# Kernel tuning notes

Measured on AMD Instinct MI355X. Metric: run time of the kernel, lower is better.

## Reference

```python
import jax, jax.numpy as jnp
import numpy as np

B, H, D, K, V, M = 64, 32, 4096, 128, 128, 4095

def setup_inputs() -> dict:
    key = jax.random.key(0)
    ks = jax.random.split(key, 7)
    return {
        "x": jax.random.normal(ks[0], (B, D), dtype=jnp.float32),
        "prev_K": jax.random.normal(ks[1], (B, M, K), dtype=jnp.float32),
        "prev_V": jax.random.normal(ks[2], (B, M, V), dtype=jnp.float32),
        "Wq": jax.random.normal(ks[3], (H, D, K), dtype=jnp.float32),
        "Wk": jax.random.normal(ks[4], (D, K), dtype=jnp.float32),
        "Wv": jax.random.normal(ks[5], (D, V), dtype=jnp.float32),
        "Wo": jax.random.normal(ks[6], (H, V, D), dtype=jnp.float32),
    }

def reference(x, prev_K, prev_V, Wq, Wk, Wv, Wo):
    # Projections
    q = jnp.einsum('bd,hdk->bhk', x, Wq)            # [b,h,k]
    k_new = jnp.einsum('bd,dk->bk', x, Wk)          # [b,k]
    v_new = jnp.einsum('bd,dv->bv', x, Wv)          # [b,v]
    Kc = jnp.concatenate([prev_K, k_new[:, None, :]], axis=1)  # [b,m+1,k]
    Vc = jnp.concatenate([prev_V, v_new[:, None, :]], axis=1)  # [b,m+1,v]
    # Shared-KV attention (MQA)
    logits = jnp.einsum('bhk,bmk->bhm', q, Kc)
    weights = jax.nn.softmax(logits, axis=-1)
    o = jnp.einsum('bhm,bmv->bhv', weights, Vc)
    y = jnp.einsum('bhv,hvd->bd', o, Wo)
    return (y, Kc, Vc)
```

## Files before the change

kernel.cpp:

```cpp
#include <hip/hip_runtime.h>
#include <stdint.h>

#define B_  64
#define H_  32
#define D_  4096
#define KD  128
#define VD  128
#define M_  4095
#define M1_ 4096
#define NCHUNK 32
#define LOG2E 1.44269504088896f

#define WS_P      0ull
#define WS_Q      4456448ull
#define WS_STATS  4718592ull
#define WS_O      4849664ull
#define WS_OPART  5111808ull

#define WAITV(n) asm volatile("s_waitcnt vmcnt(" #n ")" ::: "memory")
#define WAITVL(n) asm volatile("s_waitcnt vmcnt(" #n ") lgkmcnt(0)" ::: "memory")
#define WAITL()  asm volatile("s_waitcnt lgkmcnt(0)" ::: "memory")
#define BAR()    __builtin_amdgcn_s_barrier()

typedef __attribute__((address_space(3))) char lds_char;
typedef const __attribute__((address_space(1))) char glb_char;

__global__ __launch_bounds__(256) void k_proj_partial(
    const float* __restrict__ x, const float* __restrict__ Wq,
    const float* __restrict__ Wk, const float* __restrict__ Wv,
    float* __restrict__ P) {
  __shared__ float xs[64][256];
  const int dc = blockIdx.x;
  const int hx = blockIdx.y;
  const int t  = threadIdx.x;
  const float* xsrc = x + dc * 256;
  #pragma unroll
  for (int j = 0; j < 16; ++j) {
    int f = t + 256 * j;
    int row = f >> 6, c4 = f & 63;
    *(float4*)&xs[row][c4 * 4] =
        *(const float4*)(xsrc + (size_t)row * D_ + c4 * 4);
  }
  __syncthreads();
  const int bq = t >> 4;
  const int kg = t & 15;
  const int b0 = bq * 4;
  const float* W = (hx < H_) ? (Wq + (size_t)hx * D_ * KD)
                             : ((hx == H_) ? Wk : Wv);
  const float* wp = W + (size_t)(dc * 256) * KD + kg * 8;
  float acc[4][8];
  #pragma unroll
  for (int i = 0; i < 4; ++i)
    #pragma unroll
    for (int j = 0; j < 8; ++j) acc[i][j] = 0.f;
  #pragma unroll 8
  for (int d = 0; d < 256; ++d) {
    float4 w0 = *(const float4*)(wp + (size_t)d * KD);
    float4 w1 = *(const float4*)(wp + (size_t)d * KD + 4);
    float xv[4];
    #pragma unroll
    for (int i = 0; i < 4; ++i) xv[i] = xs[b0 + i][d];
    #pragma unroll
    for (int i = 0; i < 4; ++i) {
      acc[i][0] += xv[i] * w0.x; acc[i][1] += xv[i] * w0.y;
      acc[i][2] += xv[i] * w0.z; acc[i][3] += xv[i] * w0.w;
      acc[i][4] += xv[i] * w1.x; acc[i][5] += xv[i] * w1.y;
      acc[i][6] += xv[i] * w1.z; acc[i][7] += xv[i] * w1.w;
    }
  }
  #pragma unroll
  for (int i = 0; i < 4; ++i) {
    size_t base = ((size_t)(dc * 64 + b0 + i) * 34 + hx) * KD + kg * 8;
    *(float4*)&P[base]     = make_float4(acc[i][0], acc[i][1], acc[i][2], acc[i][3]);
    *(float4*)&P[base + 4] = make_float4(acc[i][4], acc[i][5], acc[i][6], acc[i][7]);
  }
}

__global__ __launch_bounds__(256) void k_proj_reduce(
    const float* __restrict__ P, float* __restrict__ q,
    float* __restrict__ Kc, float* __restrict__ Vc) {
  int i = blockIdx.x * 256 + threadIdx.x;
  int k = i & 127;
  int hx = (i >> 7) % 34;
  int b = i / (128 * 34);
  float s = 0.f;
  #pragma unroll
  for (int dc = 0; dc < 16; ++dc)
    s += P[(size_t)dc * (64 * 34 * 128) + (size_t)(b * 34 + hx) * 128 + k];
  if (hx < H_)       q[((size_t)b * H_ + hx) * KD + k] = s;
  else if (hx == H_) Kc[((size_t)b * M1_ + M_) * KD + k] = s;
  else               Vc[((size_t)b * M1_ + M_) * VD + k] = s;
}

__device__ __forceinline__ void stage_issue(
    const float* src, const float* app_row, float* lbuf, int m_lo, int t) {
  const int wb = t & ~63;
  #pragma unroll
  for (int j = 0; j < 4; ++j) {
    int f = j * 256 + t;
    int r = f >> 5, p = f & 31;
    int m = m_lo + r;
    int g4 = p ^ (r & 7);
    const float* gp = (m < M_) ? (src + (size_t)m * 128 + g4 * 4)
                               : (app_row + g4 * 4);
    __builtin_amdgcn_global_load_lds(
        (glb_char*)gp, (lds_char*)(lbuf + (size_t)(j * 256 + wb) * 4),
        16, 0, 0);
  }
}

__device__ __forceinline__ void copy_out(
    const float* lbuf, float* dst, int m_lo, int t) {
  const int r = t >> 3;
  const int m = m_lo + r;
  float* drow = dst + (size_t)m * 128;
  #pragma unroll
  for (int jj = 0; jj < 4; ++jj) {
    int g4 = (t & 7) + jj * 8;
    int p = g4 ^ (r & 7);
    float4 v = *(const float4*)&lbuf[(r * 32 + p) * 4];
    *(float4*)(drow + g4 * 4) = v;
  }
}

__global__ __launch_bounds__(256, 2) void k_flash(
    const float* __restrict__ prevK, const float* __restrict__ prevV,
    const float* __restrict__ q, float* __restrict__ Kc, float* __restrict__ Vc,
    float* __restrict__ o_part, float* __restrict__ stats) {
  __shared__ float buf[2][32 * 128];
  __shared__ float qs[32][128];
  __shared__ float wl[128 * 36];
  const int chunk = blockIdx.x;
  const int b = blockIdx.y;
  const int t = threadIdx.x;
  const int m0 = chunk * 128;

  const float* kbase = prevK + (size_t)b * M_ * KD;
  const float* vbase = prevV + (size_t)b * M_ * VD;
  const float* kapp  = Kc + ((size_t)b * M1_ + M_) * KD;
  const float* vapp  = Vc + ((size_t)b * M1_ + M_) * VD;
  float* kc = Kc + (size_t)b * M1_ * KD;
  float* vc = Vc + (size_t)b * M1_ * VD;

  const float* qsrc = q + (size_t)b * H_ * KD;
  float4 qv[4];
  #pragma unroll
  for (int j = 0; j < 4; ++j) {
    int f = j * 256 + t;
    qv[j] = *(const float4*)(qsrc + (size_t)(f >> 5) * KD + (f & 31) * 4);
  }
  stage_issue(kbase, kapp, buf[0], m0, t);
  #pragma unroll
  for (int j = 0; j < 4; ++j) {
    int f = j * 256 + t;
    *(float4*)&qs[f >> 5][(f & 31) * 4] = qv[j];
  }

  const int mg = t & 15, hg = t >> 4, h0 = hg * 2;
  const int v4 = t & 31, hoct = t >> 5, h0v = hoct * 4;

  float4 a0 = {0,0,0,0}, a1 = {0,0,0,0}, a2 = {0,0,0,0}, a3 = {0,0,0,0};

#define LOGITS_TILE(S, BUFI)                                                  \
  {                                                                           \
    const float* lb = buf[BUFI];                                              \
    float c00 = 0.f, c01 = 0.f, c10 = 0.f, c11 = 0.f;                         \
    const int sw = (mg & 7);                                                  \
    _Pragma("unroll 4")                                                       \
    for (int k4 = 0; k4 < 32; ++k4) {                                         \
      int p = (k4 ^ sw) * 4;                                                  \
      float4 qa = *(const float4*)&qs[h0][k4 * 4];                            \
      float4 qb = *(const float4*)&qs[h0 + 1][k4 * 4];                        \
      float4 k0v = *(const float4*)&lb[mg * 128 + p];                         \
      float4 k1v = *(const float4*)&lb[(mg + 16) * 128 + p];                  \
      c00 += qa.x*k0v.x + qa.y*k0v.y + qa.z*k0v.z + qa.w*k0v.w;               \
      c01 += qa.x*k1v.x + qa.y*k1v.y + qa.z*k1v.z + qa.w*k1v.w;               \
      c10 += qb.x*k0v.x + qb.y*k0v.y + qb.z*k0v.z + qb.w*k0v.w;               \
      c11 += qb.x*k1v.x + qb.y*k1v.y + qb.z*k1v.z + qb.w*k1v.w;               \
    }                                                                         \
    wl[((S) * 32 + mg) * 36 + h0]          = c00;                             \
    wl[((S) * 32 + mg + 16) * 36 + h0]     = c01;                             \
    wl[((S) * 32 + mg) * 36 + h0 + 1]      = c10;                             \
    wl[((S) * 32 + mg + 16) * 36 + h0 + 1] = c11;                             \
  }

#define PV_TILE(S, BUFI)                                                      \
  {                                                                           \
    const float* lb = buf[BUFI];                                              \
    _Pragma("unroll 4")                                                       \
    for (int mm = 0; mm < 32; ++mm) {                                         \
      int p = (v4 ^ (mm & 7)) * 4;                                            \
      float4 gv = *(const float4*)&lb[mm * 128 + p];                          \
      float4 w4 = *(const float4*)&wl[((S) * 32 + mm) * 36 + h0v];            \
      a0.x += w4.x*gv.x; a0.y += w4.x*gv.y; a0.z += w4.x*gv.z; a0.w += w4.x*gv.w; \
      a1.x += w4.y*gv.x; a1.y += w4.y*gv.y; a1.z += w4.y*gv.z; a1.w += w4.y*gv.w; \
      a2.x += w4.z*gv.x; a2.y += w4.z*gv.y; a2.z += w4.z*gv.z; a2.w += w4.z*gv.w; \
      a3.x += w4.w*gv.x; a3.y += w4.w*gv.y; a3.z += w4.w*gv.z; a3.w += w4.w*gv.w; \
    }                                                                         \
  }

  stage_issue(kbase, kapp, buf[1], m0 + 32, t);
  WAITVL(4); BAR();
  LOGITS_TILE(0, 0);
  copy_out(buf[0], kc, m0, t);
  WAITL(); BAR();
  stage_issue(kbase, kapp, buf[0], m0 + 64, t);
  WAITVL(8); BAR();
  LOGITS_TILE(1, 1);
  copy_out(buf[1], kc, m0 + 32, t);
  WAITL(); BAR();
  stage_issue(kbase, kapp, buf[1], m0 + 96, t);
  WAITVL(8); BAR();
  LOGITS_TILE(2, 0);
  copy_out(buf[0], kc, m0 + 64, t);
  WAITL(); BAR();
  stage_issue(vbase, vapp, buf[0], m0, t);
  WAITVL(8); BAR();
  LOGITS_TILE(3, 1);
  copy_out(buf[1], kc, m0 + 96, t);
  WAITL(); BAR();

  {
    const int h = t >> 3, s8 = t & 7;
    float vals[16];
    float mx = -3.402823466e38f;
    #pragma unroll
    for (int i = 0; i < 16; ++i) {
      vals[i] = wl[(i * 8 + s8) * 36 + h];
      mx = fmaxf(mx, vals[i]);
    }
    mx = fmaxf(mx, __shfl_xor(mx, 1));
    mx = fmaxf(mx, __shfl_xor(mx, 2));
    mx = fmaxf(mx, __shfl_xor(mx, 4));
    float sum = 0.f;
    #pragma unroll
    for (int i = 0; i < 16; ++i) {
      float e = exp2f((vals[i] - mx) * LOG2E);
      wl[(i * 8 + s8) * 36 + h] = e;
      sum += e;
    }
    sum += __shfl_xor(sum, 1);
    sum += __shfl_xor(sum, 2);
    sum += __shfl_xor(sum, 4);
    if (s8 == 0) {
      size_t sb = (((size_t)b * H_ + h) * NCHUNK + chunk) * 2;
      stats[sb]     = mx;
      stats[sb + 1] = sum;
    }
  }
  WAITL(); BAR();

  stage_issue(vbase, vapp, buf[1], m0 + 32, t);
  WAITVL(9); BAR();
  PV_TILE(0, 0);
  copy_out(buf[0], vc, m0, t);
  WAITL(); BAR();
  stage_issue(vbase, vapp, buf[0], m0 + 64, t);
  WAITVL(8); BAR();
  PV_TILE(1, 1);
  copy_out(buf[1], vc, m0 + 32, t);
  WAITL(); BAR();
  stage_issue(vbase, vapp, buf[1], m0 + 96, t);
  WAITVL(8); BAR();
  PV_TILE(2, 0);
  copy_out(buf[0], vc, m0 + 64, t);
  WAITL(); BAR();
  WAITVL(4); BAR();
  PV_TILE(3, 1);
  copy_out(buf[1], vc, m0 + 96, t);

  size_t base = ((size_t)(chunk * B_ + b) * H_ + h0v) * VD + v4 * 4;
  *(float4*)&o_part[base]          = a0;
  *(float4*)&o_part[base + VD]     = a1;
  *(float4*)&o_part[base + 2 * VD] = a2;
  *(float4*)&o_part[base + 3 * VD] = a3;
#undef LOGITS_TILE
#undef PV_TILE
}

__global__ __launch_bounds__(128) void k_combine(
    const float* __restrict__ o_part, const float* __restrict__ stats,
    float* __restrict__ o) {
  const int bh = blockIdx.x;
  const int t = threadIdx.x;
  __shared__ float st[64];
  if (t < 64) st[t] = stats[(size_t)bh * 64 + t];
  __syncthreads();
  float M = -3.402823466e38f;
  #pragma unroll
  for (int c = 0; c < NCHUNK; ++c) M = fmaxf(M, st[2 * c]);
  float wc[NCHUNK];
  float denom = 0.f;
  #pragma unroll
  for (int c = 0; c < NCHUNK; ++c) {
    float e = exp2f((st[2 * c] - M) * LOG2E);
    wc[c] = e;
    denom += st[2 * c + 1] * e;
  }
  const float inv = 1.0f / denom;
  const int b = bh >> 5, h = bh & 31;
  float acc = 0.f;
  #pragma unroll 4
  for (int c = 0; c < NCHUNK; ++c)
    acc += wc[c] * o_part[((size_t)(c * B_ + b) * H_ + h) * VD + t];
  o[(size_t)bh * VD + t] = acc * inv;
}

__global__ __launch_bounds__(256) void k_out_partial(
    const float* __restrict__ o, const float* __restrict__ Wo,
    float* __restrict__ Py) {
  __shared__ float os[64][256];
  const int dc = blockIdx.x;
  const int hvc = blockIdx.y;
  const int t = threadIdx.x;
  #pragma unroll
  for (int j = 0; j < 16; ++j) {
    int f = t + 256 * j;
    int row = f >> 6, c4 = f & 63;
    *(float4*)&os[row][c4 * 4] =
        *(const float4*)(o + (size_t)row * 4096 + hvc * 256 + c4 * 4);
  }
  __syncthreads();
  const int bq = t >> 4, dg = t & 15;
  const int b0 = bq * 4;
  const float* wp = Wo + (size_t)(hvc * 256) * D_ + dc * 128 + dg * 8;
  float acc[4][8];
  #pragma unroll
  for (int i = 0; i < 4; ++i)
    #pragma unroll
    for (int j = 0; j < 8; ++j) acc[i][j] = 0.f;
  #pragma unroll 8
  for (int hv = 0; hv < 256; ++hv) {
    float4 w0 = *(const float4*)(wp + (size_t)hv * D_);
    float4 w1 = *(const float4*)(wp + (size_t)hv * D_ + 4);
    float ov[4];
    #pragma unroll
    for (int i = 0; i < 4; ++i) ov[i] = os[b0 + i][hv];
    #pragma unroll
    for (int i = 0; i < 4; ++i) {
      acc[i][0] += ov[i] * w0.x; acc[i][1] += ov[i] * w0.y;
      acc[i][2] += ov[i] * w0.z; acc[i][3] += ov[i] * w0.w;
      acc[i][4] += ov[i] * w1.x; acc[i][5] += ov[i] * w1.y;
      acc[i][6] += ov[i] * w1.z; acc[i][7] += ov[i] * w1.w;
    }
  }
  #pragma unroll
  for (int i = 0; i < 4; ++i) {
    size_t base = ((size_t)hvc * 64 + b0 + i) * 4096 + dc * 128 + dg * 8;
    *(float4*)&Py[base]     = make_float4(acc[i][0], acc[i][1], acc[i][2], acc[i][3]);
    *(float4*)&Py[base + 4] = make_float4(acc[i][4], acc[i][5], acc[i][6], acc[i][7]);
  }
}

__global__ __launch_bounds__(256) void k_yreduce(
    const float* __restrict__ Py, float* __restrict__ y) {
  int i = blockIdx.x * 256 + threadIdx.x;
  float s = 0.f;
  #pragma unroll
  for (int c = 0; c < 16; ++c) s += Py[(size_t)c * 262144 + i];
  y[i] = s;
}

extern "C" void kernel_launch(void* const* d_in, const int* in_sizes, int n_in,
                              void* d_out, int out_size, void* d_ws, size_t ws_size,
                              hipStream_t stream) {
  const float* x     = (const float*)d_in[0];
  const float* prevK = (const float*)d_in[1];
  const float* prevV = (const float*)d_in[2];
  const float* Wq    = (const float*)d_in[3];
  const float* Wk    = (const float*)d_in[4];
  const float* Wv    = (const float*)d_in[5];
  const float* Wo    = (const float*)d_in[6];

  float* y  = (float*)d_out;
  float* Kc = y + (size_t)B_ * D_;
  float* Vc = Kc + (size_t)B_ * M1_ * KD;

  float* ws     = (float*)d_ws;
  float* P      = ws + WS_P;
  float* q      = ws + WS_Q;
  float* stats  = ws + WS_STATS;
  float* o      = ws + WS_O;
  float* o_part = ws + WS_OPART;

  k_proj_partial<<<dim3(16, 34), 256, 0, stream>>>(x, Wq, Wk, Wv, P);
  k_proj_reduce<<<1088, 256, 0, stream>>>(P, q, Kc, Vc);
  k_flash<<<dim3(32, 64), 256, 0, stream>>>(prevK, prevV, q, Kc, Vc, o_part, stats);
  k_combine<<<2048, 128, 0, stream>>>(o_part, stats, o);
  k_out_partial<<<dim3(32, 16), 256, 0, stream>>>(o, Wo, P);
  k_yreduce<<<1024, 256, 0, stream>>>(P, y);
}
```

Measured before the change: 275.4 us.

## Keep flash logits in registers, alias LDS pool, raise occupancy, pad shared tiles

The flash kernel now keeps each thread's logits in registers and does the softmax max/sum with wave shuffles, instead of writing logits to LDS and re-reading them in a separate phase. The q tile and the softmax weight tile share one LDS pool, which shrinks LDS per block, and launch bounds ask for 3 blocks per CU instead of 2. The projection and output-partial kernels pad their shared x/o tiles to 260 columns to avoid bank conflicts. In exchange it adds register pressure under the tighter launch bound, and it depends on the q region of the pool being dead before the weights overwrite it.

```diff
diff --git a/kernel.cpp b/kernel.cpp
--- a/kernel.cpp
+++ b/kernel.cpp
@@ -17,7 +17,6 @@
 #define WS_O      4849664ull
 #define WS_OPART  5111808ull
 
-#define WAITV(n) asm volatile("s_waitcnt vmcnt(" #n ")" ::: "memory")
 #define WAITVL(n) asm volatile("s_waitcnt vmcnt(" #n ") lgkmcnt(0)" ::: "memory")
 #define WAITL()  asm volatile("s_waitcnt lgkmcnt(0)" ::: "memory")
 #define BAR()    __builtin_amdgcn_s_barrier()
@@ -29,7 +28,7 @@
     const float* __restrict__ x, const float* __restrict__ Wq,
     const float* __restrict__ Wk, const float* __restrict__ Wv,
     float* __restrict__ P) {
-  __shared__ float xs[64][256];
+  __shared__ float xs[64][260];
   const int dc = blockIdx.x;
   const int hx = blockIdx.y;
   const int t  = threadIdx.x;
@@ -123,13 +122,12 @@
   }
 }
 
-__global__ __launch_bounds__(256, 2) void k_flash(
+__global__ __launch_bounds__(256, 3) void k_flash(
     const float* __restrict__ prevK, const float* __restrict__ prevV,
     const float* __restrict__ q, float* __restrict__ Kc, float* __restrict__ Vc,
     float* __restrict__ o_part, float* __restrict__ stats) {
   __shared__ float buf[2][32 * 128];
-  __shared__ float qs[32][128];
-  __shared__ float wl[128 * 36];
+  __shared__ float upool[4608];
   const int chunk = blockIdx.x;
   const int b = blockIdx.y;
   const int t = threadIdx.x;
@@ -143,23 +141,23 @@
   float* vc = Vc + (size_t)b * M1_ * VD;
 
   const float* qsrc = q + (size_t)b * H_ * KD;
-  float4 qv[4];
+  float4 qv4[4];
   #pragma unroll
   for (int j = 0; j < 4; ++j) {
     int f = j * 256 + t;
-    qv[j] = *(const float4*)(qsrc + (size_t)(f >> 5) * KD + (f & 31) * 4);
+    qv4[j] = *(const float4*)(qsrc + (size_t)(f >> 5) * KD + (f & 31) * 4);
   }
   stage_issue(kbase, kapp, buf[0], m0, t);
   #pragma unroll
   for (int j = 0; j < 4; ++j) {
     int f = j * 256 + t;
-    *(float4*)&qs[f >> 5][(f & 31) * 4] = qv[j];
+    *(float4*)&upool[(f >> 5) * 132 + (f & 31) * 4] = qv4[j];
   }
 
   const int mg = t & 15, hg = t >> 4, h0 = hg * 2;
   const int v4 = t & 31, hoct = t >> 5, h0v = hoct * 4;
 
-  float4 a0 = {0,0,0,0}, a1 = {0,0,0,0}, a2 = {0,0,0,0}, a3 = {0,0,0,0};
+  float accL0[8], accL1[8];
 
 #define LOGITS_TILE(S, BUFI)                                                  \
   {                                                                           \
@@ -169,8 +167,8 @@
     _Pragma("unroll 4")                                                       \
     for (int k4 = 0; k4 < 32; ++k4) {                                         \
       int p = (k4 ^ sw) * 4;                                                  \
-      float4 qa = *(const float4*)&qs[h0][k4 * 4];                            \
-      float4 qb = *(const float4*)&qs[h0 + 1][k4 * 4];                        \
+      float4 qa = *(const float4*)&upool[h0 * 132 + k4 * 4];                  \
+      float4 qb = *(const float4*)&upool[(h0 + 1) * 132 + k4 * 4];            \
       float4 k0v = *(const float4*)&lb[mg * 128 + p];                         \
       float4 k1v = *(const float4*)&lb[(mg + 16) * 128 + p];                  \
       c00 += qa.x*k0v.x + qa.y*k0v.y + qa.z*k0v.z + qa.w*k0v.w;               \
@@ -178,10 +176,10 @@
       c10 += qb.x*k0v.x + qb.y*k0v.y + qb.z*k0v.z + qb.w*k0v.w;               \
       c11 += qb.x*k1v.x + qb.y*k1v.y + qb.z*k1v.z + qb.w*k1v.w;               \
     }                                                                         \
-    wl[((S) * 32 + mg) * 36 + h0]          = c00;                             \
-    wl[((S) * 32 + mg + 16) * 36 + h0]     = c01;                             \
-    wl[((S) * 32 + mg) * 36 + h0 + 1]      = c10;                             \
-    wl[((S) * 32 + mg + 16) * 36 + h0 + 1] = c11;                             \
+    accL0[(S) * 2]     = c00;                                                 \
+    accL0[(S) * 2 + 1] = c01;                                                 \
+    accL1[(S) * 2]     = c10;                                                 \
+    accL1[(S) * 2 + 1] = c11;                                                 \
   }
 
 #define PV_TILE(S, BUFI)                                                      \
@@ -191,7 +189,7 @@
     for (int mm = 0; mm < 32; ++mm) {                                         \
       int p = (v4 ^ (mm & 7)) * 4;                                            \
       float4 gv = *(const float4*)&lb[mm * 128 + p];                          \
-      float4 w4 = *(const float4*)&wl[((S) * 32 + mm) * 36 + h0v];            \
+      float4 w4 = *(const float4*)&upool[((S) * 32 + mm) * 36 + h0v];         \
       a0.x += w4.x*gv.x; a0.y += w4.x*gv.y; a0.z += w4.x*gv.z; a0.w += w4.x*gv.w; \
       a1.x += w4.y*gv.x; a1.y += w4.y*gv.y; a1.z += w4.y*gv.z; a1.w += w4.y*gv.w; \
       a2.x += w4.z*gv.x; a2.y += w4.z*gv.y; a2.z += w4.z*gv.z; a2.w += w4.z*gv.w; \
@@ -204,16 +202,19 @@
   LOGITS_TILE(0, 0);
   copy_out(buf[0], kc, m0, t);
   WAITL(); BAR();
+
   stage_issue(kbase, kapp, buf[0], m0 + 64, t);
   WAITVL(8); BAR();
   LOGITS_TILE(1, 1);
   copy_out(buf[1], kc, m0 + 32, t);
   WAITL(); BAR();
+
   stage_issue(kbase, kapp, buf[1], m0 + 96, t);
   WAITVL(8); BAR();
   LOGITS_TILE(2, 0);
   copy_out(buf[0], kc, m0 + 64, t);
   WAITL(); BAR();
+
   stage_issue(vbase, vapp, buf[0], m0, t);
   WAITVL(8); BAR();
   LOGITS_TILE(3, 1);
@@ -221,50 +222,65 @@
   WAITL(); BAR();
 
   {
-    const int h = t >> 3, s8 = t & 7;
-    float vals[16];
-    float mx = -3.402823466e38f;
-    #pragma unroll
-    for (int i = 0; i < 16; ++i) {
-      vals[i] = wl[(i * 8 + s8) * 36 + h];
-      mx = fmaxf(mx, vals[i]);
-    }
-    mx = fmaxf(mx, __shfl_xor(mx, 1));
-    mx = fmaxf(mx, __shfl_xor(mx, 2));
-    mx = fmaxf(mx, __shfl_xor(mx, 4));
-    float sum = 0.f;
-    #pragma unroll
-    for (int i = 0; i < 16; ++i) {
-      float e = exp2f((vals[i] - mx) * LOG2E);
-      wl[(i * 8 + s8) * 36 + h] = e;
-      sum += e;
-    }
-    sum += __shfl_xor(sum, 1);
-    sum += __shfl_xor(sum, 2);
-    sum += __shfl_xor(sum, 4);
-    if (s8 == 0) {
-      size_t sb = (((size_t)b * H_ + h) * NCHUNK + chunk) * 2;
-      stats[sb]     = mx;
-      stats[sb + 1] = sum;
-    }
-  }
-  WAITL(); BAR();
+    float mx0 = -3.402823466e38f, mx1 = -3.402823466e38f;
+    #pragma unroll
+    for (int j = 0; j < 8; ++j) {
+      mx0 = fmaxf(mx0, accL0[j]);
+      mx1 = fmaxf(mx1, accL1[j]);
+    }
+    #pragma unroll
+    for (int off = 1; off <= 8; off <<= 1) {
+      mx0 = fmaxf(mx0, __shfl_xor(mx0, off));
+      mx1 = fmaxf(mx1, __shfl_xor(mx1, off));
+    }
+    float s0 = 0.f, s1 = 0.f;
+    #pragma unroll
+    for (int j = 0; j < 8; ++j) {
+      float e0 = exp2f((accL0[j] - mx0) * LOG2E); accL0[j] = e0; s0 += e0;
+      float e1 = exp2f((accL1[j] - mx1) * LOG2E); accL1[j] = e1; s1 += e1;
+    }
+    #pragma unroll
+    for (int off = 1; off <= 8; off <<= 1) {
+      s0 += __shfl_xor(s0, off);
+      s1 += __shfl_xor(s1, off);
+    }
+    #pragma unroll
+    for (int s = 0; s < 4; ++s)
+      #pragma unroll
+      for (int i = 0; i < 2; ++i) {
+        int m = s * 32 + mg + 16 * i;
+        upool[m * 36 + h0]     = accL0[s * 2 + i];
+        upool[m * 36 + h0 + 1] = accL1[s * 2 + i];
+      }
+    if (mg == 0) {
+      size_t sb0 = (((size_t)b * H_ + h0) * NCHUNK + chunk) * 2;
+      *(float2*)&stats[sb0] = make_float2(mx0, s0);
+      size_t sb1 = (((size_t)b * H_ + h0 + 1) * NCHUNK + chunk) * 2;
+      *(float2*)&stats[sb1] = make_float2(mx1, s1);
+    }
+  }
+  WAITL(); BAR();
+
+  float4 a0 = {0,0,0,0}, a1 = {0,0,0,0}, a2 = {0,0,0,0}, a3 = {0,0,0,0};
 
   stage_issue(vbase, vapp, buf[1], m0 + 32, t);
-  WAITVL(9); BAR();
+  WAITVL(10); BAR();
   PV_TILE(0, 0);
   copy_out(buf[0], vc, m0, t);
   WAITL(); BAR();
+
   stage_issue(vbase, vapp, buf[0], m0 + 64, t);
   WAITVL(8); BAR();
   PV_TILE(1, 1);
   copy_out(buf[1], vc, m0 + 32, t);
   WAITL(); BAR();
+
   stage_issue(vbase, vapp, buf[1], m0 + 96, t);
   WAITVL(8); BAR();
   PV_TILE(2, 0);
   copy_out(buf[0], vc, m0 + 64, t);
   WAITL(); BAR();
+
   WAITVL(4); BAR();
   PV_TILE(3, 1);
   copy_out(buf[1], vc, m0 + 96, t);
@@ -309,7 +325,7 @@
 __global__ __launch_bounds__(256) void k_out_partial(
     const float* __restrict__ o, const float* __restrict__ Wo,
     float* __restrict__ Py) {
-  __shared__ float os[64][256];
+  __shared__ float os[64][260];
   const int dc = blockIdx.x;
   const int hvc = blockIdx.y;
   const int t = threadIdx.x;
```

Result: faster. 262.0 us (-4.8%).
